# Optimization experiments

Hardware: AMD Instinct MI355X
Metric: run time of the kernel (lower is better)

The kernel has to match this reference:

```python
import jax, jax.numpy as jnp
import numpy as np

N_CORES = 64
N_QUBITS = 1024
QEMB = 256
N_EDGES = 448
BATCH = 512
NN_DIMS = (256, 512, 512, 256)


def setup_inputs() -> dict:
    key = jax.random.key(0)
    ks = jax.random.split(key, 12)
    inp = {
        "core_allocs": jax.random.randint(ks[0], (BATCH, N_QUBITS), 0, N_CORES, dtype=jnp.int32),
        "qubit_embs": jax.random.normal(ks[1], (N_QUBITS, QEMB), dtype=jnp.float32),
        "dummy_qubit_emb": jax.random.normal(ks[2], (QEMB,), dtype=jnp.float32),
        "edge_index": jax.random.randint(ks[3], (2, N_EDGES), 0, N_CORES, dtype=jnp.int32),
        "edge_weight": jax.random.uniform(ks[4], (N_EDGES,), dtype=jnp.float32),
        "W1": jax.random.normal(ks[5], (NN_DIMS[0], NN_DIMS[1]), dtype=jnp.float32) * 0.05,
        "b1": jax.random.normal(ks[6], (NN_DIMS[1],), dtype=jnp.float32) * 0.05,
        "W2": jax.random.normal(ks[7], (NN_DIMS[1], NN_DIMS[2]), dtype=jnp.float32) * 0.05,
        "b2": jax.random.normal(ks[8], (NN_DIMS[2],), dtype=jnp.float32) * 0.05,
        "W3": jax.random.normal(ks[9], (NN_DIMS[2], NN_DIMS[3]), dtype=jnp.float32) * 0.05,
        "b3": jax.random.normal(ks[10], (NN_DIMS[3],), dtype=jnp.float32) * 0.05,
    }
    return inp


def _gcn_norm(edge_index, edge_weight):
    # PyG gcn_norm: add self loops (weight 1), symmetric D^{-1/2} A D^{-1/2}.
    self_idx = jnp.arange(N_CORES, dtype=edge_index.dtype)
    row = jnp.concatenate([edge_index[0], self_idx])
    col = jnp.concatenate([edge_index[1], self_idx])
    w = jnp.concatenate([edge_weight, jnp.ones((N_CORES,), edge_weight.dtype)])
    deg = jax.ops.segment_sum(w, col, num_segments=N_CORES)  # degree at targets
    dinv = jnp.where(deg > 0, deg ** -0.5, 0.0)
    norm = dinv[row] * w * dinv[col]
    return row, col, norm


def reference(core_allocs, qubit_embs, dummy_qubit_emb, edge_index, edge_weight,
              W1, b1, W2, b2, W3, b3):
    # ---- unmixedCoreEmbs, vectorized: per-core max over assigned qubit embs,
    # dummy emb always included (cores never at capacity) ----
    def pool(alloc):  # alloc: [n_qubits] -> [n_cores, qemb]
        seg = jax.ops.segment_max(qubit_embs, alloc, num_segments=N_CORES)
        return jnp.maximum(seg, dummy_qubit_emb)  # also fixes -inf empty cores

    x = jax.vmap(pool)(core_allocs)  # [B, n_cores, qemb]

    # ---- GCNConv stack (same graph replicated per batch element) ----
    row, col, norm = _gcn_norm(edge_index, edge_weight)

    def gcn_layer(h, W, b):
        hw = h @ W  # [B, C, d_out]
        msg = hw[:, row, :] * norm[None, :, None]  # gather sources, scale
        agg = jnp.zeros((h.shape[0], N_CORES, W.shape[1]), hw.dtype).at[:, col, :].add(msg)
        return jax.nn.relu(agg + b)

    x = gcn_layer(x, W1, b1)
    x = gcn_layer(x, W2, b2)
    x = gcn_layer(x, W3, b3)
    return x  # [B, n_cores, nn_dims[-1]] (original returns this split per batch element)
```

## Files before the change

kernel.cpp:

```cpp
#include <hip/hip_runtime.h>
#include <type_traits>

typedef __attribute__((ext_vector_type(8))) short short8;
typedef __attribute__((ext_vector_type(4))) short short4v;
typedef __attribute__((ext_vector_type(2))) short short2v;
typedef __attribute__((ext_vector_type(4))) float f32x4;
typedef unsigned short u16;
typedef unsigned int u32;

#define N_EDGES 448

#define WS_ADJA 0
#define WS_ADJB 4096
#define WS_W1   8192
#define WS_W2   139264
#define WS_W3   401408
#define WS_DUM  532480
#define WS_B1   (WS_DUM + 256)
#define WS_B2   (WS_DUM + 768)
#define WS_B3   (WS_DUM + 1280)
#define WS_QE   534528
#define WS_FLAG 796672

__device__ __forceinline__ float bf2f(u16 v) {
    u32 u = ((u32)v) << 16;
    return __builtin_bit_cast(float, u);
}
__device__ __forceinline__ u16 f2bf(float f) {
    u32 u = __builtin_bit_cast(u32, f);
    u32 r = u + 0x7FFFu + ((u >> 16) & 1u);
    return (u16)(r >> 16);
}
__device__ __forceinline__ u16 f2bf_fast(float f) {
    u32 u = __builtin_bit_cast(u32, f);
    return (u16)((u + 0x8000u) >> 16);
}
__device__ __forceinline__ float ldf(const void* p, int idx, u32 isf32) {
    return isf32 ? ((const float*)p)[idx] : bf2f(((const u16*)p)[idx]);
}
__device__ __forceinline__ u16 keyb(u16 b) {
    return (u16)(b ^ ((u16)(((u16)((short)b >> 15)) >> 1)));
}
__device__ __forceinline__ u32 pkmax(u32 a, u32 b) {
    short2v x = __builtin_bit_cast(short2v, a);
    short2v y = __builtin_bit_cast(short2v, b);
    short2v r = __builtin_elementwise_max(x, y);
    return __builtin_bit_cast(u32, r);
}

__global__ __launch_bounds__(512) void prep(
    const int* __restrict__ eidx, const void* __restrict__ ew,
    const void* __restrict__ qembs, const void* __restrict__ dummy,
    const void* __restrict__ W1, const void* __restrict__ b1,
    const void* __restrict__ W2, const void* __restrict__ b2,
    const void* __restrict__ W3, const void* __restrict__ b3,
    u16* __restrict__ ws) {
    const int t = threadIdx.x, bb = blockIdx.x;
    __shared__ u32 s_isf;
    if (t < 64) {
        const u16* qs = (const u16*)qembs;
        int c = 0;
#pragma unroll
        for (int j = 0; j < 4; j++) {
            u16 v = qs[(t * 4 + j) * 2];
            u32 e = (v >> 7) & 0xFF;
            c += (e >= 100 && e <= 134) ? 1 : 0;
        }
#pragma unroll
        for (int off = 32; off > 0; off >>= 1) c += __shfl_down(c, off, 64);
        if (t == 0) s_isf = (c < 128) ? 1u : 0u;
    }
    __syncthreads();
    const u32 isf32 = s_isf;

    if (t < 128) {
        const int bw = bb * 2 + (t >> 6);
        const int tl = t & 63;
        const void* src;
        int N, K32, dst, nt, kk;
        if (bw < 256)      { src = W1; N = 512; K32 = 8;  dst = WS_W1; nt = bw / 8;          kk = bw % 8; }
        else if (bw < 768) { src = W2; N = 512; K32 = 16; dst = WS_W2; nt = (bw - 256) / 16; kk = (bw - 256) % 16; }
        else               { src = W3; N = 256; K32 = 16; dst = WS_W3; nt = (bw - 768) / 16; kk = (bw - 768) % 16; }
        const int col = nt * 16 + (tl & 15);
        const int krow = kk * 32 + (tl >> 4) * 8;
        u16 v[8];
#pragma unroll
        for (int j = 0; j < 8; j++) v[j] = f2bf(ldf(src, (krow + j) * N + col, isf32));
        u16* o = ws + dst + (nt * K32 + kk) * 512 + tl * 8;
#pragma unroll
        for (int j = 0; j < 8; j++) o[j] = v[j];
    }
    if (t >= 256) {
        const int base = bb * 512 + (t - 256) * 2;
        ws[WS_QE + base]     = keyb(f2bf(ldf(qembs, base, isf32)));
        ws[WS_QE + base + 1] = keyb(f2bf(ldf(qembs, base + 1, isf32)));
    }
    if (bb == 1) {
#pragma unroll
        for (int j = 0; j < 4; j++) {
            int i = t + j * 512;
            if (i < 1792) {
                u16 o;
                if (i < 256)       o = keyb(f2bf(ldf(dummy, i, isf32)));
                else if (i < 768)  o = f2bf(ldf(b1, i - 256, isf32));
                else if (i < 1280) o = f2bf(ldf(b2, i - 768, isf32));
                else               o = f2bf(ldf(b3, i - 1280, isf32));
                ws[WS_DUM + i] = o;
            }
        }
    }
    if (bb == 0) {
        __shared__ float A[4096];
        __shared__ float deg[64];
        __shared__ float dinv[64];
        __shared__ int er[N_EDGES];
        __shared__ int ec[N_EDGES];
        __shared__ float ewf[N_EDGES];
        if (t < N_EDGES) {
            er[t] = eidx[t];
            ec[t] = eidx[N_EDGES + t];
            ewf[t] = ldf(ew, t, isf32);
        }
        if (t < 64) deg[t] = 1.0f;
        for (int i = t; i < 4096; i += 512) A[i] = 0.f;
        __syncthreads();
        if (t < N_EDGES) atomicAdd(&deg[ec[t]], ewf[t]);
        __syncthreads();
        if (t < 64) dinv[t] = 1.0f / sqrtf(deg[t]);
        __syncthreads();
        if (t < N_EDGES) atomicAdd(&A[ec[t] * 64 + er[t]], dinv[er[t]] * ewf[t] * dinv[ec[t]]);
        __syncthreads();
        if (t < 64) A[t * 64 + t] += dinv[t] * dinv[t];
        __syncthreads();
        for (int i = t; i < 4096; i += 512) {
            int chunk = i >> 9, m = (i >> 3) & 63, j = i & 7;
            ws[WS_ADJA + i] = f2bf(A[m * 64 + chunk * 8 + j]);
        }
        for (int i = t; i < 4096; i += 512) {
            int chunk = i >> 9, l = (i >> 3) & 63, j = i & 7;
            int ntc = chunk >> 1, kk = chunk & 1;
            int k = kk * 32 + (l >> 4) * 8 + j;
            int c2 = ntc * 16 + (l & 15);
            ws[WS_ADJB + i] = f2bf(A[c2 * 64 + k]);
        }
        if (t == 0) *(u32*)(ws + WS_FLAG) = isf32;
    }
}

__global__ __launch_bounds__(512, 4) void fused(
    const int* __restrict__ allocs, const u16* __restrict__ ws,
    void* __restrict__ out) {

    __shared__ __align__(16) u16 BUF[64 * 512];
    __shared__ __align__(16) u16 ADJB_S[4096];

    const int t = threadIdx.x, bb = blockIdx.x;
    const int wave = t >> 6, lane = t & 63, quad = lane >> 4, nl = lane & 15;
    const u32 isf32 = *(const u32*)(ws + WS_FLAG);

    *(uint4*)(ADJB_S + t * 8) = *(const uint4*)(ws + WS_ADJB + t * 8);

    {
        int* LIST = (int*)(BUF + 16384);
        int* CNT  = LIST + 1024;
        int* SST  = CNT + 64;
        int* WOF  = SST + 64;
        if (t < 64) CNT[t] = 0;
        __syncthreads();
        const int c0 = allocs[bb * 1024 + t];
        const int c1 = allocs[bb * 1024 + 512 + t];
        atomicAdd(&CNT[c0], 1);
        atomicAdd(&CNT[c1], 1);
        __syncthreads();
        if (t < 64) {
            int v = CNT[t], s = v;
#pragma unroll
            for (int off = 1; off < 64; off <<= 1) {
                int u = __shfl_up(s, off, 64);
                if (t >= off) s += u;
            }
            SST[t] = s - v;
            WOF[t] = s - v;
        }
        __syncthreads();
        {
            int p0 = atomicAdd(&WOF[c0], 1); LIST[p0] = t;
            int p1 = atomicAdd(&WOF[c1], 1); LIST[p1] = 512 + t;
        }
        __syncthreads();
        const u16* wsq = ws + WS_QE;
        const uint2 dk = *(const uint2*)(ws + WS_DUM + lane * 4);
        for (int i = 0; i < 8; i++) {
            const int c = wave * 8 + i;
            const int L = CNT[c], S = SST[c];
            u32 m0 = dk.x, m1 = dk.y;
            int j = 0;
            for (; j + 4 <= L; j += 4) {
                const int q0 = LIST[S + j],     q1 = LIST[S + j + 1];
                const int q2 = LIST[S + j + 2], q3 = LIST[S + j + 3];
                uint2 ra = *(const uint2*)(wsq + q0 * 256 + lane * 4);
                uint2 rb = *(const uint2*)(wsq + q1 * 256 + lane * 4);
                uint2 rc = *(const uint2*)(wsq + q2 * 256 + lane * 4);
                uint2 rd = *(const uint2*)(wsq + q3 * 256 + lane * 4);
                m0 = pkmax(pkmax(m0, ra.x), pkmax(rb.x, rc.x));
                m1 = pkmax(pkmax(m1, ra.y), pkmax(rb.y, rc.y));
                m0 = pkmax(m0, rd.x);
                m1 = pkmax(m1, rd.y);
            }
            for (; j < L; j++) {
                const int q = LIST[S + j];
                uint2 r = *(const uint2*)(wsq + q * 256 + lane * 4);
                m0 = pkmax(m0, r.x);
                m1 = pkmax(m1, r.y);
            }
            short4v p;
            p[0] = (short)keyb((u16)(m0 & 0xffffu));
            p[1] = (short)keyb((u16)(m0 >> 16));
            p[2] = (short)keyb((u16)(m1 & 0xffffu));
            p[3] = (short)keyb((u16)(m1 >> 16));
            *(short4v*)(BUF + (lane >> 1) * 512 + c * 8 + (lane & 1) * 4) = p;
        }
    }
    __syncthreads();

    auto layerT = [&](auto K32c, const u16* __restrict__ W, const u16* __restrict__ bias) {
        constexpr int K32 = decltype(K32c)::value;
        const int s0 = wave * 4;
        u16* scr = BUF + (wave * 8 + 6) * 512;
        f32x4 acc[4][4];
#pragma unroll
        for (int s = 0; s < 4; s++)
#pragma unroll
            for (int rt = 0; rt < 4; rt++) acc[s][rt] = f32x4{0.f, 0.f, 0.f, 0.f};
#pragma unroll
        for (int kk = 0; kk < K32; kk++) {
            short8 a[4], bch[4];
#pragma unroll
            for (int rt = 0; rt < 4; rt++)
                a[rt] = *(const short8*)(BUF + (kk * 4 + quad) * 512 + (rt * 16 + nl) * 8);
#pragma unroll
            for (int s = 0; s < 4; s++)
                bch[s] = *(const short8*)(W + ((s0 + s) * K32 + kk) * 512 + lane * 8);
#pragma unroll
            for (int s = 0; s < 4; s++)
#pragma unroll
                for (int rt = 0; rt < 4; rt++)
                    acc[s][rt] = __builtin_amdgcn_mfma_f32_16x16x32_bf16(a[rt], bch[s], acc[s][rt], 0, 0, 0);
        }
        __syncthreads();
#pragma unroll
        for (int s = 0; s < 4; s++) {
            const int nt = s0 + s;
            f32x4 agg[4];
#pragma unroll
            for (int ntc = 0; ntc < 4; ntc++) agg[ntc] = f32x4{0.f, 0.f, 0.f, 0.f};
#pragma unroll
            for (int h = 0; h < 2; h++) {
#pragma unroll
                for (int r2 = 0; r2 < 2; r2++) {
                    f32x4 v = acc[s][2 * h + r2];
                    short4v p;
#pragma unroll
                    for (int rr = 0; rr < 4; rr++) p[rr] = (short)f2bf_fast(v[rr]);
                    *(short4v*)(scr + nl * 40 + r2 * 16 + quad * 4) = p;
                }
                short8 hwf = *(const short8*)(scr + nl * 40 + quad * 8);
#pragma unroll
                for (int ntc = 0; ntc < 4; ntc++) {
                    short8 bfrag = *(const short8*)(ADJB_S + (ntc * 2 + h) * 512 + lane * 8);
                    agg[ntc] = __builtin_amdgcn_mfma_f32_16x16x32_bf16(hwf, bfrag, agg[ntc], 0, 0, 0);
                }
            }
            float bv[4];
#pragma unroll
            for (int rr = 0; rr < 4; rr++) bv[rr] = bf2f(bias[nt * 16 + quad * 4 + rr]);
#pragma unroll
            for (int ntc = 0; ntc < 4; ntc++) {
                short4v p;
#pragma unroll
                for (int rr = 0; rr < 4; rr++)
                    p[rr] = (short)f2bf_fast(fmaxf(agg[ntc][rr] + bv[rr], 0.f));
                *(short4v*)(BUF + (nt * 2 + (quad >> 1)) * 512 + (ntc * 16 + nl) * 8 + (quad & 1) * 4) = p;
            }
        }
        __syncthreads();
    };

    auto layer3 = [&](const u16* __restrict__ W) {
        f32x4 acc[2][4];
#pragma unroll
        for (int s = 0; s < 2; s++)
#pragma unroll
            for (int rt = 0; rt < 4; rt++) acc[s][rt] = f32x4{0.f, 0.f, 0.f, 0.f};
#pragma unroll
        for (int kk = 0; kk < 16; kk++) {
            short8 a[4], bch[2];
#pragma unroll
            for (int rt = 0; rt < 4; rt++)
                a[rt] = *(const short8*)(BUF + (kk * 4 + quad) * 512 + (rt * 16 + nl) * 8);
#pragma unroll
            for (int s = 0; s < 2; s++)
                bch[s] = *(const short8*)(W + ((wave * 2 + s) * 16 + kk) * 512 + lane * 8);
#pragma unroll
            for (int s = 0; s < 2; s++)
#pragma unroll
                for (int rt = 0; rt < 4; rt++)
                    acc[s][rt] = __builtin_amdgcn_mfma_f32_16x16x32_bf16(a[rt], bch[s], acc[s][rt], 0, 0, 0);
        }
        __syncthreads();
        u16* scr = BUF + 16384 + wave * 640;
#pragma unroll
        for (int s = 0; s < 2; s++) {
            const int nt = wave * 2 + s;
#pragma unroll
            for (int h = 0; h < 2; h++) {
#pragma unroll
                for (int r2 = 0; r2 < 2; r2++) {
                    f32x4 v = acc[s][2 * h + r2];
                    short4v p;
#pragma unroll
                    for (int rr = 0; rr < 4; rr++) p[rr] = (short)f2bf_fast(v[rr]);
                    *(short4v*)(scr + nl * 40 + r2 * 16 + quad * 4) = p;
                }
                short8 hwf = *(const short8*)(scr + nl * 40 + quad * 8);
                *(short8*)(BUF + (nt * 2 + h) * 512 + lane * 8) = hwf;
            }
        }
        __syncthreads();
    };

    layerT(std::integral_constant<int, 8>{},  ws + WS_W1, ws + WS_B1);
    layerT(std::integral_constant<int, 16>{}, ws + WS_W2, ws + WS_B2);
    layer3(ws + WS_W3);

    {
        const int rt2 = wave & 3, nt0 = (wave >> 2) * 8;
        short8 aA[2];
#pragma unroll
        for (int h = 0; h < 2; h++)
            aA[h] = *(const short8*)(ws + WS_ADJA + (h * 4 + quad) * 512 + (rt2 * 16 + nl) * 8);
        f32x4 accv[8];
#pragma unroll
        for (int ni = 0; ni < 8; ni++) {
            const int nt = nt0 + ni;
            short8 b0v = *(const short8*)(BUF + (nt * 2 + 0) * 512 + lane * 8);
            short8 b1v = *(const short8*)(BUF + (nt * 2 + 1) * 512 + lane * 8);
            f32x4 a = f32x4{0.f, 0.f, 0.f, 0.f};
            a = __builtin_amdgcn_mfma_f32_16x16x32_bf16(aA[0], b0v, a, 0, 0, 0);
            a = __builtin_amdgcn_mfma_f32_16x16x32_bf16(aA[1], b1v, a, 0, 0, 0);
            accv[ni] = a;
        }
        __syncthreads();
        float* Hf = (float*)BUF;
#pragma unroll
        for (int ni = 0; ni < 8; ni++) {
            const int n = (nt0 + ni) * 16 + nl;
            const float bv = bf2f(ws[WS_B3 + n]);
#pragma unroll
            for (int rr = 0; rr < 4; rr++) {
                const int m2 = rt2 * 16 + quad * 4 + rr;
                Hf[m2 * 256 + n] = fmaxf(accv[ni][rr] + bv, 0.f);
            }
        }
        __syncthreads();
        if (isf32) {
            float4* outv = (float4*)((float*)out + (size_t)bb * 16384);
            const float4* Hv = (const float4*)Hf;
#pragma unroll
            for (int p4 = 0; p4 < 8; p4++) outv[p4 * 512 + t] = Hv[p4 * 512 + t];
        } else {
            u16* outu = (u16*)out + (size_t)bb * 16384;
#pragma unroll
            for (int p4 = 0; p4 < 8; p4++) {
                const int idx = (p4 * 512 + t) * 4;
                float4 v = *(const float4*)(Hf + idx);
                short4v pk;
                pk[0] = (short)f2bf_fast(v.x); pk[1] = (short)f2bf_fast(v.y);
                pk[2] = (short)f2bf_fast(v.z); pk[3] = (short)f2bf_fast(v.w);
                *(short4v*)(outu + idx) = pk;
            }
        }
    }
}

extern "C" void kernel_launch(void* const* d_in, const int* in_sizes, int n_in,
                              void* d_out, int out_size, void* d_ws, size_t ws_size,
                              hipStream_t stream) {
    const int* allocs = (const int*)d_in[0];
    const void* qembs = d_in[1];
    const void* dummy = d_in[2];
    const int* eidx   = (const int*)d_in[3];
    const void* ew    = d_in[4];
    const void* W1 = d_in[5];
    const void* b1 = d_in[6];
    const void* W2 = d_in[7];
    const void* b2 = d_in[8];
    const void* W3 = d_in[9];
    const void* b3 = d_in[10];
    u16* ws = (u16*)d_ws;

    prep<<<512, 512, 0, stream>>>(eidx, ew, qembs, dummy, W1, b1, W2, b2, W3, b3, ws);
    fused<<<512, 512, 0, stream>>>(allocs, ws, d_out);
}
```

Baseline: 151.2 us.

## Double fused kernel block to 1024 threads and keep adjacency fragments in registers

The fused kernel now launches 1024 threads (16 waves) per batch element instead of 512, so each wave handles half as many cores in pooling, half as many output tiles in each GEMM layer, and half as many output stores. The adjacency B-fragments are now loaded once from global memory into registers per wave instead of being staged in shared memory and reread per tile. The aim is more latency hiding and less per-wave serial work, at the cost of higher register pressure under launch_bounds(1024,4) and heavier barrier synchronisation across more waves. The scratch regions in BUF are re-partitioned to match the wave count.

```diff
diff --git a/kernel.cpp b/kernel.cpp
--- a/kernel.cpp
+++ b/kernel.cpp
@@ -147,18 +147,15 @@
     }
 }
 
-__global__ __launch_bounds__(512, 4) void fused(
+__global__ __launch_bounds__(1024, 4) void fused(
     const int* __restrict__ allocs, const u16* __restrict__ ws,
     void* __restrict__ out) {
 
     __shared__ __align__(16) u16 BUF[64 * 512];
-    __shared__ __align__(16) u16 ADJB_S[4096];
 
     const int t = threadIdx.x, bb = blockIdx.x;
     const int wave = t >> 6, lane = t & 63, quad = lane >> 4, nl = lane & 15;
     const u32 isf32 = *(const u32*)(ws + WS_FLAG);
-
-    *(uint4*)(ADJB_S + t * 8) = *(const uint4*)(ws + WS_ADJB + t * 8);
 
     {
         int* LIST = (int*)(BUF + 16384);
@@ -167,10 +164,8 @@
         int* WOF  = SST + 64;
         if (t < 64) CNT[t] = 0;
         __syncthreads();
-        const int c0 = allocs[bb * 1024 + t];
-        const int c1 = allocs[bb * 1024 + 512 + t];
-        atomicAdd(&CNT[c0], 1);
-        atomicAdd(&CNT[c1], 1);
+        const int myc = allocs[bb * 1024 + t];
+        atomicAdd(&CNT[myc], 1);
         __syncthreads();
         if (t < 64) {
             int v = CNT[t], s = v;
@@ -184,14 +179,14 @@
         }
         __syncthreads();
         {
-            int p0 = atomicAdd(&WOF[c0], 1); LIST[p0] = t;
-            int p1 = atomicAdd(&WOF[c1], 1); LIST[p1] = 512 + t;
+            int pos = atomicAdd(&WOF[myc], 1);
+            LIST[pos] = t;
         }
         __syncthreads();
         const u16* wsq = ws + WS_QE;
         const uint2 dk = *(const uint2*)(ws + WS_DUM + lane * 4);
-        for (int i = 0; i < 8; i++) {
-            const int c = wave * 8 + i;
+        for (int i = 0; i < 4; i++) {
+            const int c = wave * 4 + i;
             const int L = CNT[c], S = SST[c];
             u32 m0 = dk.x, m1 = dk.y;
             int j = 0;
@@ -223,33 +218,40 @@
     }
     __syncthreads();
 
+    short8 adjB[4][2];
+#pragma unroll
+    for (int ntc = 0; ntc < 4; ntc++)
+#pragma unroll
+        for (int h = 0; h < 2; h++)
+            adjB[ntc][h] = *(const short8*)(ws + WS_ADJB + (ntc * 2 + h) * 512 + lane * 8);
+
     auto layerT = [&](auto K32c, const u16* __restrict__ W, const u16* __restrict__ bias) {
         constexpr int K32 = decltype(K32c)::value;
-        const int s0 = wave * 4;
-        u16* scr = BUF + (wave * 8 + 6) * 512;
-        f32x4 acc[4][4];
-#pragma unroll
-        for (int s = 0; s < 4; s++)
+        const int s0 = wave * 2;
+        u16* scr = BUF + (wave * 4 + 2) * 512;
+        f32x4 acc[2][4];
+#pragma unroll
+        for (int s = 0; s < 2; s++)
 #pragma unroll
             for (int rt = 0; rt < 4; rt++) acc[s][rt] = f32x4{0.f, 0.f, 0.f, 0.f};
 #pragma unroll
         for (int kk = 0; kk < K32; kk++) {
-            short8 a[4], bch[4];
+            short8 a[4], bch[2];
 #pragma unroll
             for (int rt = 0; rt < 4; rt++)
                 a[rt] = *(const short8*)(BUF + (kk * 4 + quad) * 512 + (rt * 16 + nl) * 8);
 #pragma unroll
-            for (int s = 0; s < 4; s++)
+            for (int s = 0; s < 2; s++)
                 bch[s] = *(const short8*)(W + ((s0 + s) * K32 + kk) * 512 + lane * 8);
 #pragma unroll
-            for (int s = 0; s < 4; s++)
+            for (int s = 0; s < 2; s++)
 #pragma unroll
                 for (int rt = 0; rt < 4; rt++)
                     acc[s][rt] = __builtin_amdgcn_mfma_f32_16x16x32_bf16(a[rt], bch[s], acc[s][rt], 0, 0, 0);
         }
         __syncthreads();
 #pragma unroll
-        for (int s = 0; s < 4; s++) {
+        for (int s = 0; s < 2; s++) {
             const int nt = s0 + s;
             f32x4 agg[4];
 #pragma unroll
@@ -266,10 +268,8 @@
                 }
                 short8 hwf = *(const short8*)(scr + nl * 40 + quad * 8);
 #pragma unroll
-                for (int ntc = 0; ntc < 4; ntc++) {
-                    short8 bfrag = *(const short8*)(ADJB_S + (ntc * 2 + h) * 512 + lane * 8);
-                    agg[ntc] = __builtin_amdgcn_mfma_f32_16x16x32_bf16(hwf, bfrag, agg[ntc], 0, 0, 0);
-                }
+                for (int ntc = 0; ntc < 4; ntc++)
+                    agg[ntc] = __builtin_amdgcn_mfma_f32_16x16x32_bf16(hwf, adjB[ntc][h], agg[ntc], 0, 0, 0);
             }
             float bv[4];
 #pragma unroll
@@ -287,44 +287,35 @@
     };
 
     auto layer3 = [&](const u16* __restrict__ W) {
-        f32x4 acc[2][4];
-#pragma unroll
-        for (int s = 0; s < 2; s++)
-#pragma unroll
-            for (int rt = 0; rt < 4; rt++) acc[s][rt] = f32x4{0.f, 0.f, 0.f, 0.f};
+        const int nt = wave;
+        f32x4 acc[4];
+#pragma unroll
+        for (int rt = 0; rt < 4; rt++) acc[rt] = f32x4{0.f, 0.f, 0.f, 0.f};
 #pragma unroll
         for (int kk = 0; kk < 16; kk++) {
-            short8 a[4], bch[2];
+            short8 a[4];
 #pragma unroll
             for (int rt = 0; rt < 4; rt++)
                 a[rt] = *(const short8*)(BUF + (kk * 4 + quad) * 512 + (rt * 16 + nl) * 8);
-#pragma unroll
-            for (int s = 0; s < 2; s++)
-                bch[s] = *(const short8*)(W + ((wave * 2 + s) * 16 + kk) * 512 + lane * 8);
-#pragma unroll
-            for (int s = 0; s < 2; s++)
-#pragma unroll
-                for (int rt = 0; rt < 4; rt++)
-                    acc[s][rt] = __builtin_amdgcn_mfma_f32_16x16x32_bf16(a[rt], bch[s], acc[s][rt], 0, 0, 0);
+            short8 bch = *(const short8*)(W + (nt * 16 + kk) * 512 + lane * 8);
+#pragma unroll
+            for (int rt = 0; rt < 4; rt++)
+                acc[rt] = __builtin_amdgcn_mfma_f32_16x16x32_bf16(a[rt], bch, acc[rt], 0, 0, 0);
         }
         __syncthreads();
         u16* scr = BUF + 16384 + wave * 640;
 #pragma unroll
-        for (int s = 0; s < 2; s++) {
-            const int nt = wave * 2 + s;
-#pragma unroll
-            for (int h = 0; h < 2; h++) {
-#pragma unroll
-                for (int r2 = 0; r2 < 2; r2++) {
-                    f32x4 v = acc[s][2 * h + r2];
-                    short4v p;
-#pragma unroll
-                    for (int rr = 0; rr < 4; rr++) p[rr] = (short)f2bf_fast(v[rr]);
-                    *(short4v*)(scr + nl * 40 + r2 * 16 + quad * 4) = p;
-                }
-                short8 hwf = *(const short8*)(scr + nl * 40 + quad * 8);
-                *(short8*)(BUF + (nt * 2 + h) * 512 + lane * 8) = hwf;
-            }
+        for (int h = 0; h < 2; h++) {
+#pragma unroll
+            for (int r2 = 0; r2 < 2; r2++) {
+                f32x4 v = acc[2 * h + r2];
+                short4v p;
+#pragma unroll
+                for (int rr = 0; rr < 4; rr++) p[rr] = (short)f2bf_fast(v[rr]);
+                *(short4v*)(scr + nl * 40 + r2 * 16 + quad * 4) = p;
+            }
+            short8 hwf = *(const short8*)(scr + nl * 40 + quad * 8);
+            *(short8*)(BUF + (nt * 2 + h) * 512 + lane * 8) = hwf;
         }
         __syncthreads();
     };
@@ -334,14 +325,14 @@
     layer3(ws + WS_W3);
 
     {
-        const int rt2 = wave & 3, nt0 = (wave >> 2) * 8;
+        const int rt2 = wave & 3, nt0 = (wave >> 2) * 4;
         short8 aA[2];
 #pragma unroll
         for (int h = 0; h < 2; h++)
             aA[h] = *(const short8*)(ws + WS_ADJA + (h * 4 + quad) * 512 + (rt2 * 16 + nl) * 8);
-        f32x4 accv[8];
-#pragma unroll
-        for (int ni = 0; ni < 8; ni++) {
+        f32x4 accv[4];
+#pragma unroll
+        for (int ni = 0; ni < 4; ni++) {
             const int nt = nt0 + ni;
             short8 b0v = *(const short8*)(BUF + (nt * 2 + 0) * 512 + lane * 8);
             short8 b1v = *(const short8*)(BUF + (nt * 2 + 1) * 512 + lane * 8);
@@ -353,7 +344,7 @@
         __syncthreads();
         float* Hf = (float*)BUF;
 #pragma unroll
-        for (int ni = 0; ni < 8; ni++) {
+        for (int ni = 0; ni < 4; ni++) {
             const int n = (nt0 + ni) * 16 + nl;
             const float bv = bf2f(ws[WS_B3 + n]);
 #pragma unroll
@@ -367,12 +358,12 @@
             float4* outv = (float4*)((float*)out + (size_t)bb * 16384);
             const float4* Hv = (const float4*)Hf;
 #pragma unroll
-            for (int p4 = 0; p4 < 8; p4++) outv[p4 * 512 + t] = Hv[p4 * 512 + t];
+            for (int p4 = 0; p4 < 4; p4++) outv[p4 * 1024 + t] = Hv[p4 * 1024 + t];
         } else {
             u16* outu = (u16*)out + (size_t)bb * 16384;
 #pragma unroll
-            for (int p4 = 0; p4 < 8; p4++) {
-                const int idx = (p4 * 512 + t) * 4;
+            for (int p4 = 0; p4 < 4; p4++) {
+                const int idx = (p4 * 1024 + t) * 4;
                 float4 v = *(const float4*)(Hf + idx);
                 short4v pk;
                 pk[0] = (short)f2bf_fast(v.x); pk[1] = (short)f2bf_fast(v.y);
@@ -400,5 +391,5 @@
     u16* ws = (u16*)d_ws;
 
     prep<<<512, 512, 0, stream>>>(eidx, ew, qembs, dummy, W1, b1, W2, b2, W3, b3, ws);
-    fused<<<512, 512, 0, stream>>>(allocs, ws, d_out);
-}
+    fused<<<512, 1024, 0, stream>>>(allocs, ws, d_out);
+}
```

After: 148.8 us. No clear change (-1.6%).
